# Optimization experiments

Hardware: AMD Instinct MI355X
Metric: run time of the kernel (lower is better)

Reference implementation:

```python
import jax, jax.numpy as jnp
import numpy as np

N, C, M, P, FL = 2, 512, 8, 1, 4
SPATIAL = [(100, 100), (50, 50), (25, 25), (13, 13)]
S = sum(h * w for h, w in SPATIAL)
CM = C // M


def grid_sample_zeros(im, grid):
    """torch.nn.functional.grid_sample, bilinear, padding_mode='zeros', align_corners=False.
    im: (B, Cc, H, W); grid: (B, Hg, Wg, 2) with grid[...,0]=x, grid[...,1]=y in [-1,1].
    Returns (B, Cc, Hg, Wg)."""
    B, Cc, H, W = im.shape
    Hg, Wg = grid.shape[1], grid.shape[2]
    x = (grid[..., 0] + 1.0) * (W * 0.5) - 0.5
    y = (grid[..., 1] + 1.0) * (H * 0.5) - 0.5
    x0f = jnp.floor(x)
    y0f = jnp.floor(y)
    wx1 = x - x0f
    wy1 = y - y0f
    wx0 = 1.0 - wx1
    wy0 = 1.0 - wy1
    x0 = x0f.astype(jnp.int32)
    y0 = y0f.astype(jnp.int32)
    flat = im.reshape(B, Cc, H * W)

    def gather(ix, iy):
        valid = ((ix >= 0) & (ix < W) & (iy >= 0) & (iy < H)).astype(im.dtype)
        idx = jnp.clip(iy, 0, H - 1) * W + jnp.clip(ix, 0, W - 1)  # (B,Hg,Wg)
        idx = jnp.broadcast_to(idx.reshape(B, 1, Hg * Wg), (B, Cc, Hg * Wg))
        v = jnp.take_along_axis(flat, idx, axis=2).reshape(B, Cc, Hg, Wg)
        return v * valid[:, None]

    out = (gather(x0, y0) * (wx0 * wy0)[:, None]
           + gather(x0 + 1, y0) * (wx1 * wy0)[:, None]
           + gather(x0, y0 + 1) * (wx0 * wy1)[:, None]
           + gather(x0 + 1, y0 + 1) * (wx1 * wy1)[:, None])
    return out


def setup_inputs() -> dict:
    key = jax.random.key(0)
    ks = jax.random.split(key, 8)
    x = jax.random.normal(ks[0], (N, C, S), jnp.float32)
    pos = jax.random.normal(ks[1], (N, C, S), jnp.float32)
    key_padding_mask = jnp.zeros((N, S), jnp.bool_)
    # valid (W,H) per level; no padding -> full size, scale 1
    valid_sizes = jnp.broadcast_to(
        jnp.array([[w, h] for (h, w) in SPATIAL], jnp.float32)[None], (N, FL, 2))
    valid_scales = jnp.ones((N, FL, 2), jnp.float32)
    s = 1.0 / np.sqrt(C)
    Wv = (jax.random.normal(ks[2], (C, C), jnp.float32) * s)
    bv = jnp.zeros((C,), jnp.float32)
    Wloc = jax.random.normal(ks[3], (M * FL * P * 2, C), jnp.float32) * 0.01
    # torch bias init: head-direction grid, channel layout (M, F, P, 2)
    grid_init = np.array([-1, -1, -1, 0, -1, 1, 0, -1, 0, 1, 1, -1, 1, 0, 1, 1],
                         np.float32).reshape(M, 1, 1, 2)
    grid_init = np.tile(grid_init, (1, FL, P, 1))
    for i in range(P):
        grid_init[:, :, i, :] *= (i + 1)
    bloc = jnp.asarray(grid_init.reshape(-1))
    Ww = jax.random.normal(ks[4], (M * FL * P, C), jnp.float32) * 0.01
    bw = jnp.zeros((M * FL * P,), jnp.float32)
    Wo = (jax.random.normal(ks[5], (C, C), jnp.float32) * s)
    bo = jnp.zeros((C,), jnp.float32)
    scale = jnp.ones((C,), jnp.float32)
    return dict(x=x, pos=pos, key_padding_mask=key_padding_mask,
                valid_sizes=valid_sizes, valid_scales=valid_scales,
                Wv=Wv, bv=bv, Wloc=Wloc, bloc=bloc, Ww=Ww, bw=bw,
                Wo=Wo, bo=bo, scale=scale)


def reference(x, pos, key_padding_mask, valid_sizes, valid_scales,
              Wv, bv, Wloc, bloc, Ww, bw, Wo, bo, scale):
    mask = key_padding_mask[:, None, :]  # (N,1,S)
    x_pos = jnp.where(mask, 0.0, x + pos)
    value = jnp.einsum('oc,ncs->nos', Wv, x) + bv[:, None]
    value = jnp.where(mask, 0.0, value)

    # per-level value maps, split heads: (N*M, C/M, H, W)
    values, cur = [], 0
    for (H, W) in SPATIAL:
        values.append(value[..., cur:cur + H * W].reshape(N * M, CM, H, W))
        cur += H * W

    vs = jnp.repeat(valid_sizes, M, axis=0)          # (NM, F, 2) = repeat_interleave
    vc2 = jnp.repeat(2.0 * valid_scales, M, axis=0)  # (NM, F, 2)

    outs, cur = [], 0
    for lvl, (H, W) in enumerate(SPATIAL):
        L = H * W
        xp = x_pos[..., cur:cur + L]  # (N, C, L)
        cur += L
        # 1x1 convs == per-token linears
        off = jnp.einsum('oc,ncl->nol', Wloc, xp) + bloc[:, None]
        off = off.reshape(N * M, FL, P, 2, L).transpose(0, 1, 2, 4, 3)  # (NM,F,P,L,2)
        w = jnp.einsum('oc,ncl->nol', Ww, xp) + bw[:, None]
        w = jax.nn.softmax(w.reshape(N * M, 1, FL * P, L), axis=2)
        # pixel-center grid of the query level, (L,2) as (x,y)
        ys, xs = jnp.meshgrid(jnp.arange(H, dtype=jnp.float32) + 0.5,
                              jnp.arange(W, dtype=jnp.float32) + 0.5, indexing='ij')
        pre = jnp.stack([xs, ys], -1).reshape(L, 2)
        sc = (vc2 / vs[:, lvl:lvl + 1])[:, :, None, None, :]  # (NM,F,1,1,2)
        grids = off * sc + (pre[None, None, None] * sc - 1.0)  # (NM,F,P,L,2)
        samples = jnp.concatenate(
            [grid_sample_zeros(values[f], grids[:, f]) for f in range(FL)], axis=2)  # (NM,CM,F*P,L)
        out = jnp.sum(samples * w, axis=2).reshape(N, C, L)
        out = jnp.einsum('oc,ncl->nol', Wo, out) + bo[:, None]
        outs.append(out)
    return jnp.concatenate(outs, axis=-1) * scale[None, :, None]
```

## Files before the change

### kernel.cpp

```cpp
#include <hip/hip_runtime.h>
#include <math.h>

#define TOT_S   13294
#define NBATCH  2
#define CCH     512
#define MHEAD   8
#define PITCH   40

typedef short     short8  __attribute__((ext_vector_type(8)));
typedef float     f32x4   __attribute__((ext_vector_type(4)));
typedef unsigned short u16x8 __attribute__((ext_vector_type(8)));
typedef unsigned short u16x4 __attribute__((ext_vector_type(4)));

__device__ __forceinline__ unsigned short f2bf(float f) {
    union { float f; unsigned int u; } v; v.f = f;
    unsigned int r = v.u + 0x7fffu + ((v.u >> 16) & 1u);
    return (unsigned short)(r >> 16);
}
__device__ __forceinline__ float bf2f(unsigned short h) {
    union { unsigned int u; float f; } v; v.u = ((unsigned int)h) << 16;
    return v.f;
}

__global__ void cast_f32_bf16(const float* __restrict__ src,
                              unsigned short* __restrict__ dst, int n4)
{
    const int i = blockIdx.x * blockDim.x + threadIdx.x;
    if (i < n4) {
        const float4 v = *(const float4*)(src + (size_t)i * 4);
        u16x4 o;
        o[0] = f2bf(v.x); o[1] = f2bf(v.y); o[2] = f2bf(v.z); o[3] = f2bf(v.w);
        *(u16x4*)(dst + (size_t)i * 4) = o;
    }
}

__global__ __launch_bounds__(256)
void cast_transpose(const float* __restrict__ x, const float* __restrict__ pos,
                    const unsigned char* __restrict__ mask,
                    unsigned short* __restrict__ xbt,
                    unsigned short* __restrict__ xpbt)
{
    const int lane = threadIdx.x;
    const int n = blockIdx.z;
    const int s = blockIdx.x * 64 + lane;
    if (s >= TOT_S) return;
    const int cb = (blockIdx.y * 4 + threadIdx.y) * 8;
    const float* xp = x   + ((size_t)n * CCH + cb) * TOT_S + s;
    const float* pp = pos + ((size_t)n * CCH + cb) * TOT_S + s;
    const bool mk = mask[(size_t)n * TOT_S + s] != 0;
    u16x8 vx, vp;
#pragma unroll
    for (int j = 0; j < 8; ++j) {
        const float a = xp[(size_t)j * TOT_S];
        const float b = pp[(size_t)j * TOT_S];
        vx[j] = f2bf(a);
        vp[j] = mk ? (unsigned short)0 : f2bf(a + b);
    }
    const size_t o = ((size_t)n * TOT_S + s) * CCH + cb;
    *(u16x8*)(xbt + o)  = vx;
    *(u16x8*)(xpbt + o) = vp;
}

__global__ __launch_bounds__(256)
void gemm_value_mfma(const unsigned short* __restrict__ Wb,
                     const unsigned short* __restrict__ Act,
                     const float* __restrict__ bv,
                     const unsigned char* __restrict__ mask,
                     unsigned short* __restrict__ valb)
{
    __shared__ unsigned short Wl[128 * PITCH];
    __shared__ unsigned short Al[128 * PITCH];
    const int n  = blockIdx.z;
    const int ob = blockIdx.y * 128;
    const int sb = blockIdx.x * 128;
    const int tid = threadIdx.x;
    const int r   = tid >> 1;
    const int seg = (tid & 1) * 16;
    const unsigned short* wsrc = Wb + ((size_t)(ob + r)) * CCH + seg;
    const int sr = min(sb + r, TOT_S - 1);
    const unsigned short* asrc = Act + ((size_t)n * TOT_S + sr) * CCH + seg;
    unsigned short* wdst = &Wl[r * PITCH + seg];
    unsigned short* adst = &Al[r * PITCH + seg];

    const int wave = tid >> 6, lane = tid & 63;
    const int m0 = (wave & 1) * 64, n0 = (wave >> 1) * 64;
    const int row16 = lane & 15, q = lane >> 4;

    u16x8 w0 = *(const u16x8*)(wsrc);
    u16x8 w1 = *(const u16x8*)(wsrc + 8);
    u16x8 a0 = *(const u16x8*)(asrc);
    u16x8 a1 = *(const u16x8*)(asrc + 8);

    f32x4 acc[4][4] = {};
    for (int k0 = 0; k0 < CCH; k0 += 32) {
        *(u16x8*)wdst = w0; *(u16x8*)(wdst + 8) = w1;
        *(u16x8*)adst = a0; *(u16x8*)(adst + 8) = a1;
        __syncthreads();
        if (k0 + 32 < CCH) {
            w0 = *(const u16x8*)(wsrc + k0 + 32);
            w1 = *(const u16x8*)(wsrc + k0 + 40);
            a0 = *(const u16x8*)(asrc + k0 + 32);
            a1 = *(const u16x8*)(asrc + k0 + 40);
        }
        short8 af[4], bfr[4];
#pragma unroll
        for (int mt = 0; mt < 4; ++mt)
            af[mt] = *(const short8*)&Wl[(m0 + mt * 16 + row16) * PITCH + q * 8];
#pragma unroll
        for (int nt = 0; nt < 4; ++nt)
            bfr[nt] = *(const short8*)&Al[(n0 + nt * 16 + row16) * PITCH + q * 8];
#pragma unroll
        for (int mt = 0; mt < 4; ++mt)
#pragma unroll
            for (int nt = 0; nt < 4; ++nt)
                acc[mt][nt] = __builtin_amdgcn_mfma_f32_16x16x32_bf16(
                    af[mt], bfr[nt], acc[mt][nt], 0, 0, 0);
        __syncthreads();
    }

#pragma unroll
    for (int nt = 0; nt < 4; ++nt) {
        const int s = sb + n0 + nt * 16 + row16;
        if (s >= TOT_S) continue;
        const float msk = mask[(size_t)n * TOT_S + s] ? 0.f : 1.f;
        unsigned short* orow = valb + ((size_t)n * TOT_S + s) * CCH + ob + m0;
#pragma unroll
        for (int mt = 0; mt < 4; ++mt) {
            const f32x4 bvv = *(const f32x4*)(bv + ob + m0 + mt * 16 + q * 4);
            const f32x4 a = acc[mt][nt];
            u16x4 ov;
            ov[0] = f2bf((a[0] + bvv[0]) * msk);
            ov[1] = f2bf((a[1] + bvv[1]) * msk);
            ov[2] = f2bf((a[2] + bvv[2]) * msk);
            ov[3] = f2bf((a[3] + bvv[3]) * msk);
            *(u16x4*)(orow + mt * 16 + q * 4) = ov;
        }
    }
}

__global__ __launch_bounds__(256)
void gemm_offw_mfma(const unsigned short* __restrict__ Wlb,
                    const unsigned short* __restrict__ Wwb,
                    const float* __restrict__ bloc, const float* __restrict__ bw,
                    const unsigned short* __restrict__ Act,
                    float* __restrict__ offw)
{
    __shared__ unsigned short Wl[128 * PITCH];
    __shared__ unsigned short Al[128 * PITCH];
    const int n  = blockIdx.z;
    const int sb = blockIdx.x * 128;
    const int tid = threadIdx.x;
    const int r   = tid >> 1;
    const int seg = (tid & 1) * 16;
    const bool wzero = (r >= 96);
    const unsigned short* wsrc =
        (r < 64) ? (Wlb + (size_t)r * CCH + seg)
                 : (Wwb + (size_t)((r < 96 ? r : 95) - 64) * CCH + seg);
    const int sr = min(sb + r, TOT_S - 1);
    const unsigned short* asrc = Act + ((size_t)n * TOT_S + sr) * CCH + seg;
    unsigned short* wdst = &Wl[r * PITCH + seg];
    unsigned short* adst = &Al[r * PITCH + seg];

    const int wave = tid >> 6, lane = tid & 63;
    const int m0 = (wave & 1) * 64, n0 = (wave >> 1) * 64;
    const int row16 = lane & 15, q = lane >> 4;

    u16x8 w0 = {}, w1 = {};
    if (!wzero) { w0 = *(const u16x8*)(wsrc); w1 = *(const u16x8*)(wsrc + 8); }
    u16x8 a0 = *(const u16x8*)(asrc);
    u16x8 a1 = *(const u16x8*)(asrc + 8);

    f32x4 acc[4][4] = {};
    for (int k0 = 0; k0 < CCH; k0 += 32) {
        *(u16x8*)wdst = w0; *(u16x8*)(wdst + 8) = w1;
        *(u16x8*)adst = a0; *(u16x8*)(adst + 8) = a1;
        __syncthreads();
        if (k0 + 32 < CCH) {
            if (!wzero) {
                w0 = *(const u16x8*)(wsrc + k0 + 32);
                w1 = *(const u16x8*)(wsrc + k0 + 40);
            }
            a0 = *(const u16x8*)(asrc + k0 + 32);
            a1 = *(const u16x8*)(asrc + k0 + 40);
        }
        short8 af[4], bfr[4];
#pragma unroll
        for (int mt = 0; mt < 4; ++mt)
            af[mt] = *(const short8*)&Wl[(m0 + mt * 16 + row16) * PITCH + q * 8];
#pragma unroll
        for (int nt = 0; nt < 4; ++nt)
            bfr[nt] = *(const short8*)&Al[(n0 + nt * 16 + row16) * PITCH + q * 8];
#pragma unroll
        for (int mt = 0; mt < 4; ++mt)
#pragma unroll
            for (int nt = 0; nt < 4; ++nt)
                acc[mt][nt] = __builtin_amdgcn_mfma_f32_16x16x32_bf16(
                    af[mt], bfr[nt], acc[mt][nt], 0, 0, 0);
        __syncthreads();
    }

#pragma unroll
    for (int nt = 0; nt < 4; ++nt) {
        const int s = sb + n0 + nt * 16 + row16;
        if (s >= TOT_S) continue;
        float* orow = offw + ((size_t)n * TOT_S + s) * 96;
#pragma unroll
        for (int mt = 0; mt < 4; ++mt) {
            const int o = m0 + mt * 16 + q * 4;
            if (o < 96) {
                const float* bsrc = (o < 64) ? (bloc + o) : (bw + o - 64);
                const f32x4 bb = *(const f32x4*)bsrc;
                f32x4 v = acc[mt][nt];
                v[0] += bb[0]; v[1] += bb[1]; v[2] += bb[2]; v[3] += bb[3];
                *(f32x4*)(orow + o) = v;
            }
        }
    }
}

__global__ __launch_bounds__(256)
void sample_attn(const unsigned short* __restrict__ value,
                 const float* __restrict__ offw,
                 const float* __restrict__ vsizes,
                 const float* __restrict__ vscales,
                 unsigned short* __restrict__ samp)
{
    const int lane = threadIdx.x;
    const int item = blockIdx.x * blockDim.y + threadIdx.y;
    const int total = NBATCH * TOT_S;
    if (item >= total) return;
    const int s = item % TOT_S;
    const int n = item / TOT_S;
    const int m = lane >> 3;

    int lvl; float prex, prey;
    if (s < 10000)      { lvl = 0; const int l = s;         const int qq = l / 100; prey = qq + 0.5f; prex = (l - qq * 100) + 0.5f; }
    else if (s < 12500) { lvl = 1; const int l = s - 10000; const int qq = l / 50;  prey = qq + 0.5f; prex = (l - qq * 50)  + 0.5f; }
    else if (s < 13125) { lvl = 2; const int l = s - 12500; const int qq = l / 25;  prey = qq + 0.5f; prex = (l - qq * 25)  + 0.5f; }
    else                { lvl = 3; const int l = s - 13125; const int qq = l / 13;  prey = qq + 0.5f; prex = (l - qq * 13)  + 0.5f; }

    const float* ow = offw + ((size_t)n * TOT_S + s) * 96;

    const float w0 = ow[64 + m * 4 + 0], w1 = ow[64 + m * 4 + 1];
    const float w2 = ow[64 + m * 4 + 2], w3 = ow[64 + m * 4 + 3];
    const float mx = fmaxf(fmaxf(w0, w1), fmaxf(w2, w3));
    const float e0 = expf(w0 - mx), e1 = expf(w1 - mx), e2 = expf(w2 - mx), e3 = expf(w3 - mx);
    const float inv = 1.f / (e0 + e1 + e2 + e3);
    const float wgt[4] = { e0 * inv, e1 * inv, e2 * inv, e3 * inv };

    const int HS[4]  = { 100, 50, 25, 13 };
    const int WS[4]  = { 100, 50, 25, 13 };
    const int CUR[4] = { 0, 10000, 12500, 13125 };

    const float invsx = 1.f / vsizes[((n * 4) + lvl) * 2 + 0];
    const float invsy = 1.f / vsizes[((n * 4) + lvl) * 2 + 1];
    const unsigned short* vbase = value + (size_t)n * TOT_S * CCH + lane * 8;

    float acc[8] = {};
#pragma unroll
    for (int f = 0; f < 4; ++f) {
        const float offx = ow[(m * 4 + f) * 2 + 0];
        const float offy = ow[(m * 4 + f) * 2 + 1];
        const float scx = 2.f * vscales[((n * 4) + f) * 2 + 0] * invsx;
        const float scy = 2.f * vscales[((n * 4) + f) * 2 + 1] * invsy;
        const int Wf = WS[f], Hf = HS[f], cf = CUR[f];
        const float xi = (offx + prex) * scx * (Wf * 0.5f) - 0.5f;
        const float yi = (offy + prey) * scy * (Hf * 0.5f) - 0.5f;
        const float x0f = floorf(xi), y0f = floorf(yi);
        const float wx1 = xi - x0f, wy1 = yi - y0f;
        const float wx0 = 1.f - wx1, wy0 = 1.f - wy1;
        const int x0 = (int)x0f, y0 = (int)y0f;
        const bool xin0 = (x0 >= 0) && (x0 < Wf);
        const bool xin1 = (x0 + 1 >= 0) && (x0 + 1 < Wf);
        const bool yin0 = (y0 >= 0) && (y0 < Hf);
        const bool yin1 = (y0 + 1 >= 0) && (y0 + 1 < Hf);
        const float cw00 = (xin0 && yin0) ? wgt[f] * wx0 * wy0 : 0.f;
        const float cw10 = (xin1 && yin0) ? wgt[f] * wx1 * wy0 : 0.f;
        const float cw01 = (xin0 && yin1) ? wgt[f] * wx0 * wy1 : 0.f;
        const float cw11 = (xin1 && yin1) ? wgt[f] * wx1 * wy1 : 0.f;
        const int x0c = min(max(x0, 0), Wf - 1);
        const int x1c = min(max(x0 + 1, 0), Wf - 1);
        const int y0c = min(max(y0, 0), Hf - 1);
        const int y1c = min(max(y0 + 1, 0), Hf - 1);
        const unsigned short* row0 = vbase + (size_t)(cf + y0c * Wf) * CCH;
        const unsigned short* row1 = vbase + (size_t)(cf + y1c * Wf) * CCH;
        const u16x8 v00 = *(const u16x8*)(row0 + (size_t)x0c * CCH);
        const u16x8 v10 = *(const u16x8*)(row0 + (size_t)x1c * CCH);
        const u16x8 v01 = *(const u16x8*)(row1 + (size_t)x0c * CCH);
        const u16x8 v11 = *(const u16x8*)(row1 + (size_t)x1c * CCH);
#pragma unroll
        for (int j = 0; j < 8; ++j) {
            acc[j] += cw00 * bf2f(v00[j]) + cw10 * bf2f(v10[j])
                    + cw01 * bf2f(v01[j]) + cw11 * bf2f(v11[j]);
        }
    }

    u16x8 ov;
#pragma unroll
    for (int j = 0; j < 8; ++j) ov[j] = f2bf(acc[j]);
    *(u16x8*)(samp + ((size_t)n * TOT_S + s) * CCH + lane * 8) = ov;
}

__global__ __launch_bounds__(256)
void gemm_out_mfma(const unsigned short* __restrict__ Wob,
                   const unsigned short* __restrict__ Sampb,
                   const float* __restrict__ bo, const float* __restrict__ scale,
                   float* __restrict__ out)
{
    __shared__ unsigned short Sl[128 * PITCH];
    __shared__ unsigned short Wl[128 * PITCH];
    const int n  = blockIdx.z;
    const int ob = blockIdx.y * 128;
    const int sb = blockIdx.x * 128;
    const int tid = threadIdx.x;
    const int r   = tid >> 1;
    const int seg = (tid & 1) * 16;
    const int sr = min(sb + r, TOT_S - 1);
    const unsigned short* ssrc = Sampb + ((size_t)n * TOT_S + sr) * CCH + seg;
    const unsigned short* wsrc = Wob + ((size_t)(ob + r)) * CCH + seg;
    unsigned short* sdst = &Sl[r * PITCH + seg];
    unsigned short* wdst = &Wl[r * PITCH + seg];

    const int wave = tid >> 6, lane = tid & 63;
    const int m0 = (wave & 1) * 64, n0 = (wave >> 1) * 64;
    const int row16 = lane & 15, q = lane >> 4;

    u16x8 s0v = *(const u16x8*)(ssrc);
    u16x8 s1v = *(const u16x8*)(ssrc + 8);
    u16x8 w0v = *(const u16x8*)(wsrc);
    u16x8 w1v = *(const u16x8*)(wsrc + 8);

    f32x4 acc[4][4] = {};
    for (int k0 = 0; k0 < CCH; k0 += 32) {
        *(u16x8*)sdst = s0v; *(u16x8*)(sdst + 8) = s1v;
        *(u16x8*)wdst = w0v; *(u16x8*)(wdst + 8) = w1v;
        __syncthreads();
        if (k0 + 32 < CCH) {
            s0v = *(const u16x8*)(ssrc + k0 + 32);
            s1v = *(const u16x8*)(ssrc + k0 + 40);
            w0v = *(const u16x8*)(wsrc + k0 + 32);
            w1v = *(const u16x8*)(wsrc + k0 + 40);
        }
        short8 af[4], bfr[4];
#pragma unroll
        for (int mt = 0; mt < 4; ++mt)
            af[mt] = *(const short8*)&Sl[(m0 + mt * 16 + row16) * PITCH + q * 8];
#pragma unroll
        for (int nt = 0; nt < 4; ++nt)
            bfr[nt] = *(const short8*)&Wl[(n0 + nt * 16 + row16) * PITCH + q * 8];
#pragma unroll
        for (int mt = 0; mt < 4; ++mt)
#pragma unroll
            for (int nt = 0; nt < 4; ++nt)
                acc[mt][nt] = __builtin_amdgcn_mfma_f32_16x16x32_bf16(
                    af[mt], bfr[nt], acc[mt][nt], 0, 0, 0);
        __syncthreads();
    }

#pragma unroll
    for (int nt = 0; nt < 4; ++nt) {
        const int o = ob + n0 + nt * 16 + row16;
        const float bo_ = bo[o];
        const float sc_ = scale[o];
        float* orow = out + ((size_t)n * CCH + o) * (size_t)TOT_S;
#pragma unroll
        for (int mt = 0; mt < 4; ++mt) {
            const int s0 = sb + m0 + mt * 16 + q * 4;
            const f32x4 a = acc[mt][nt];
            if (s0 + 3 < TOT_S) {
                float2 v0 = make_float2((a[0] + bo_) * sc_, (a[1] + bo_) * sc_);
                float2 v1 = make_float2((a[2] + bo_) * sc_, (a[3] + bo_) * sc_);
                *(float2*)(orow + s0) = v0;
                *(float2*)(orow + s0 + 2) = v1;
            } else {
                for (int i = 0; i < 4; ++i)
                    if (s0 + i < TOT_S) orow[s0 + i] = (a[i] + bo_) * sc_;
            }
        }
    }
}

extern "C" void kernel_launch(void* const* d_in, const int* in_sizes, int n_in,
                              void* d_out, int out_size, void* d_ws, size_t ws_size,
                              hipStream_t stream)
{
    const float* x     = (const float*)d_in[0];
    const float* pos   = (const float*)d_in[1];
    const unsigned char* mask = (const unsigned char*)d_in[2];
    const float* vsz   = (const float*)d_in[3];
    const float* vsc   = (const float*)d_in[4];
    const float* Wv    = (const float*)d_in[5];
    const float* bv    = (const float*)d_in[6];
    const float* Wloc  = (const float*)d_in[7];
    const float* bloc  = (const float*)d_in[8];
    const float* Ww    = (const float*)d_in[9];
    const float* bw    = (const float*)d_in[10];
    const float* Wo    = (const float*)d_in[11];
    const float* bo    = (const float*)d_in[12];
    const float* scale = (const float*)d_in[13];
    float* out = (float*)d_out;

    const size_t SC = (size_t)TOT_S * CCH;
    unsigned short* valb  = (unsigned short*)d_ws;
    unsigned short* sampb = valb  + 2 * SC;
    unsigned short* xbt   = sampb + 2 * SC;
    unsigned short* xpbt  = xbt   + 2 * SC;
    float* offw = (float*)(xpbt + 2 * SC);
    unsigned short* wvb = (unsigned short*)(offw + 2 * (size_t)TOT_S * 96);
    unsigned short* wob = wvb + 512 * 512;
    unsigned short* wlb = wob + 512 * 512;
    unsigned short* wwb = wlb + 64 * 512;

    cast_f32_bf16<<<256, 256, 0, stream>>>(Wv,   wvb, 512 * 512 / 4);
    cast_f32_bf16<<<256, 256, 0, stream>>>(Wo,   wob, 512 * 512 / 4);
    cast_f32_bf16<<<32,  256, 0, stream>>>(Wloc, wlb, 64 * 512 / 4);
    cast_f32_bf16<<<16,  256, 0, stream>>>(Ww,   wwb, 32 * 512 / 4);

    cast_transpose<<<dim3((TOT_S + 63) / 64, 16, NBATCH), dim3(64, 4), 0, stream>>>(
        x, pos, mask, xbt, xpbt);

    const int sTiles = (TOT_S + 127) / 128;

    gemm_value_mfma<<<dim3(sTiles, CCH / 128, NBATCH), 256, 0, stream>>>(
        wvb, xbt, bv, mask, valb);
    gemm_offw_mfma<<<dim3(sTiles, 1, NBATCH), 256, 0, stream>>>(
        wlb, wwb, bloc, bw, xpbt, offw);

    const int items = NBATCH * TOT_S;
    sample_attn<<<(items + 3) / 4, dim3(64, 4), 0, stream>>>(valb, offw, vsz, vsc, sampb);

    gemm_out_mfma<<<dim3(sTiles, CCH / 128, NBATCH), 256, 0, stream>>>(
        wob, sampb, bo, scale, out);
}
```

Baseline: 314.2 us.

## Fuse fp32-to-bf16 cast and transpose into value and offset GEMM loaders

Removes the separate cast_transpose kernel and has the value and offset/weight GEMMs read fp32 x and pos directly from channel-major layout. They convert to bf16 on the fly and transpose into shared memory. This drops the bf16 transposed intermediate buffers and their write/read round trip. The cost is that the value GEMM rereads fp32 x once per output-channel tile (4x), and the shared-memory stores are narrower and may bank-conflict.

```diff
diff --git a/kernel.cpp b/kernel.cpp
--- a/kernel.cpp
+++ b/kernel.cpp
@@ -35,35 +35,8 @@
 }
 
 __global__ __launch_bounds__(256)
-void cast_transpose(const float* __restrict__ x, const float* __restrict__ pos,
-                    const unsigned char* __restrict__ mask,
-                    unsigned short* __restrict__ xbt,
-                    unsigned short* __restrict__ xpbt)
-{
-    const int lane = threadIdx.x;
-    const int n = blockIdx.z;
-    const int s = blockIdx.x * 64 + lane;
-    if (s >= TOT_S) return;
-    const int cb = (blockIdx.y * 4 + threadIdx.y) * 8;
-    const float* xp = x   + ((size_t)n * CCH + cb) * TOT_S + s;
-    const float* pp = pos + ((size_t)n * CCH + cb) * TOT_S + s;
-    const bool mk = mask[(size_t)n * TOT_S + s] != 0;
-    u16x8 vx, vp;
-#pragma unroll
-    for (int j = 0; j < 8; ++j) {
-        const float a = xp[(size_t)j * TOT_S];
-        const float b = pp[(size_t)j * TOT_S];
-        vx[j] = f2bf(a);
-        vp[j] = mk ? (unsigned short)0 : f2bf(a + b);
-    }
-    const size_t o = ((size_t)n * TOT_S + s) * CCH + cb;
-    *(u16x8*)(xbt + o)  = vx;
-    *(u16x8*)(xpbt + o) = vp;
-}
-
-__global__ __launch_bounds__(256)
 void gemm_value_mfma(const unsigned short* __restrict__ Wb,
-                     const unsigned short* __restrict__ Act,
+                     const float* __restrict__ X,
                      const float* __restrict__ bv,
                      const unsigned char* __restrict__ mask,
                      unsigned short* __restrict__ valb)
@@ -74,13 +47,18 @@
     const int ob = blockIdx.y * 128;
     const int sb = blockIdx.x * 128;
     const int tid = threadIdx.x;
+
     const int r   = tid >> 1;
     const int seg = (tid & 1) * 16;
     const unsigned short* wsrc = Wb + ((size_t)(ob + r)) * CCH + seg;
-    const int sr = min(sb + r, TOT_S - 1);
-    const unsigned short* asrc = Act + ((size_t)n * TOT_S + sr) * CCH + seg;
     unsigned short* wdst = &Wl[r * PITCH + seg];
-    unsigned short* adst = &Al[r * PITCH + seg];
+
+    const int kr = tid & 7;
+    const int sq = tid >> 3;
+    const int sl = sq * 4;
+    const int sg = sb + sl;
+    const float* Xn = X + (size_t)n * CCH * TOT_S;
+    const bool fast = (sg + 3 < TOT_S);
 
     const int wave = tid >> 6, lane = tid & 63;
     const int m0 = (wave & 1) * 64, n0 = (wave >> 1) * 64;
@@ -88,19 +66,42 @@
 
     u16x8 w0 = *(const u16x8*)(wsrc);
     u16x8 w1 = *(const u16x8*)(wsrc + 8);
-    u16x8 a0 = *(const u16x8*)(asrc);
-    u16x8 a1 = *(const u16x8*)(asrc + 8);
+    f32x4 xv[4];
+#pragma unroll
+    for (int j = 0; j < 4; ++j) {
+        const size_t roff = (size_t)(kr * 4 + j) * TOT_S;
+        if (fast) xv[j] = *(const f32x4*)(Xn + roff + sg);
+        else {
+#pragma unroll
+            for (int i = 0; i < 4; ++i)
+                xv[j][i] = Xn[roff + min(sg + i, TOT_S - 1)];
+        }
+    }
 
     f32x4 acc[4][4] = {};
     for (int k0 = 0; k0 < CCH; k0 += 32) {
         *(u16x8*)wdst = w0; *(u16x8*)(wdst + 8) = w1;
-        *(u16x8*)adst = a0; *(u16x8*)(adst + 8) = a1;
+#pragma unroll
+        for (int i = 0; i < 4; ++i) {
+            u16x4 t;
+            t[0] = f2bf(xv[0][i]); t[1] = f2bf(xv[1][i]);
+            t[2] = f2bf(xv[2][i]); t[3] = f2bf(xv[3][i]);
+            *(u16x4*)&Al[(sl + i) * PITCH + kr * 4] = t;
+        }
         __syncthreads();
         if (k0 + 32 < CCH) {
             w0 = *(const u16x8*)(wsrc + k0 + 32);
             w1 = *(const u16x8*)(wsrc + k0 + 40);
-            a0 = *(const u16x8*)(asrc + k0 + 32);
-            a1 = *(const u16x8*)(asrc + k0 + 40);
+#pragma unroll
+            for (int j = 0; j < 4; ++j) {
+                const size_t roff = (size_t)(k0 + 32 + kr * 4 + j) * TOT_S;
+                if (fast) xv[j] = *(const f32x4*)(Xn + roff + sg);
+                else {
+#pragma unroll
+                    for (int i = 0; i < 4; ++i)
+                        xv[j][i] = Xn[roff + min(sg + i, TOT_S - 1)];
+                }
+            }
         }
         short8 af[4], bfr[4];
 #pragma unroll
@@ -142,7 +143,8 @@
 void gemm_offw_mfma(const unsigned short* __restrict__ Wlb,
                     const unsigned short* __restrict__ Wwb,
                     const float* __restrict__ bloc, const float* __restrict__ bw,
-                    const unsigned short* __restrict__ Act,
+                    const float* __restrict__ X, const float* __restrict__ POS,
+                    const unsigned char* __restrict__ mask,
                     float* __restrict__ offw)
 {
     __shared__ unsigned short Wl[128 * PITCH];
@@ -150,16 +152,26 @@
     const int n  = blockIdx.z;
     const int sb = blockIdx.x * 128;
     const int tid = threadIdx.x;
+
     const int r   = tid >> 1;
     const int seg = (tid & 1) * 16;
     const bool wzero = (r >= 96);
     const unsigned short* wsrc =
         (r < 64) ? (Wlb + (size_t)r * CCH + seg)
                  : (Wwb + (size_t)((r < 96 ? r : 95) - 64) * CCH + seg);
-    const int sr = min(sb + r, TOT_S - 1);
-    const unsigned short* asrc = Act + ((size_t)n * TOT_S + sr) * CCH + seg;
     unsigned short* wdst = &Wl[r * PITCH + seg];
-    unsigned short* adst = &Al[r * PITCH + seg];
+
+    const int kr = tid & 7;
+    const int sq = tid >> 3;
+    const int sl = sq * 4;
+    const int sg = sb + sl;
+    const float* Xn = X   + (size_t)n * CCH * TOT_S;
+    const float* Pn = POS + (size_t)n * CCH * TOT_S;
+    const bool fast = (sg + 3 < TOT_S);
+    float mkf[4];
+#pragma unroll
+    for (int i = 0; i < 4; ++i)
+        mkf[i] = mask[(size_t)n * TOT_S + min(sg + i, TOT_S - 1)] ? 0.f : 1.f;
 
     const int wave = tid >> 6, lane = tid & 63;
     const int m0 = (wave & 1) * 64, n0 = (wave >> 1) * 64;
@@ -167,21 +179,56 @@
 
     u16x8 w0 = {}, w1 = {};
     if (!wzero) { w0 = *(const u16x8*)(wsrc); w1 = *(const u16x8*)(wsrc + 8); }
-    u16x8 a0 = *(const u16x8*)(asrc);
-    u16x8 a1 = *(const u16x8*)(asrc + 8);
+    f32x4 xv[4];
+#pragma unroll
+    for (int j = 0; j < 4; ++j) {
+        const size_t roff = (size_t)(kr * 4 + j) * TOT_S;
+        if (fast) {
+            const f32x4 a = *(const f32x4*)(Xn + roff + sg);
+            const f32x4 b = *(const f32x4*)(Pn + roff + sg);
+#pragma unroll
+            for (int i = 0; i < 4; ++i) xv[j][i] = (a[i] + b[i]) * mkf[i];
+        } else {
+#pragma unroll
+            for (int i = 0; i < 4; ++i) {
+                const int si = min(sg + i, TOT_S - 1);
+                xv[j][i] = (Xn[roff + si] + Pn[roff + si]) * mkf[i];
+            }
+        }
+    }
 
     f32x4 acc[4][4] = {};
     for (int k0 = 0; k0 < CCH; k0 += 32) {
         *(u16x8*)wdst = w0; *(u16x8*)(wdst + 8) = w1;
-        *(u16x8*)adst = a0; *(u16x8*)(adst + 8) = a1;
+#pragma unroll
+        for (int i = 0; i < 4; ++i) {
+            u16x4 t;
+            t[0] = f2bf(xv[0][i]); t[1] = f2bf(xv[1][i]);
+            t[2] = f2bf(xv[2][i]); t[3] = f2bf(xv[3][i]);
+            *(u16x4*)&Al[(sl + i) * PITCH + kr * 4] = t;
+        }
         __syncthreads();
         if (k0 + 32 < CCH) {
             if (!wzero) {
                 w0 = *(const u16x8*)(wsrc + k0 + 32);
                 w1 = *(const u16x8*)(wsrc + k0 + 40);
             }
-            a0 = *(const u16x8*)(asrc + k0 + 32);
-            a1 = *(const u16x8*)(asrc + k0 + 40);
+#pragma unroll
+            for (int j = 0; j < 4; ++j) {
+                const size_t roff = (size_t)(k0 + 32 + kr * 4 + j) * TOT_S;
+                if (fast) {
+                    const f32x4 a = *(const f32x4*)(Xn + roff + sg);
+                    const f32x4 b = *(const f32x4*)(Pn + roff + sg);
+#pragma unroll
+                    for (int i = 0; i < 4; ++i) xv[j][i] = (a[i] + b[i]) * mkf[i];
+                } else {
+#pragma unroll
+                    for (int i = 0; i < 4; ++i) {
+                        const int si = min(sg + i, TOT_S - 1);
+                        xv[j][i] = (Xn[roff + si] + Pn[roff + si]) * mkf[i];
+                    }
+                }
+            }
         }
         short8 af[4], bfr[4];
 #pragma unroll
@@ -403,9 +450,7 @@
     const size_t SC = (size_t)TOT_S * CCH;
     unsigned short* valb  = (unsigned short*)d_ws;
     unsigned short* sampb = valb  + 2 * SC;
-    unsigned short* xbt   = sampb + 2 * SC;
-    unsigned short* xpbt  = xbt   + 2 * SC;
-    float* offw = (float*)(xpbt + 2 * SC);
+    float* offw = (float*)(sampb + 2 * SC);
     unsigned short* wvb = (unsigned short*)(offw + 2 * (size_t)TOT_S * 96);
     unsigned short* wob = wvb + 512 * 512;
     unsigned short* wlb = wob + 512 * 512;
@@ -416,15 +461,12 @@
     cast_f32_bf16<<<32,  256, 0, stream>>>(Wloc, wlb, 64 * 512 / 4);
     cast_f32_bf16<<<16,  256, 0, stream>>>(Ww,   wwb, 32 * 512 / 4);
 
-    cast_transpose<<<dim3((TOT_S + 63) / 64, 16, NBATCH), dim3(64, 4), 0, stream>>>(
-        x, pos, mask, xbt, xpbt);
-
     const int sTiles = (TOT_S + 127) / 128;
 
     gemm_value_mfma<<<dim3(sTiles, CCH / 128, NBATCH), 256, 0, stream>>>(
-        wvb, xbt, bv, mask, valb);
+        wvb, x, bv, mask, valb);
     gemm_offw_mfma<<<dim3(sTiles, 1, NBATCH), 256, 0, stream>>>(
-        wlb, wwb, bloc, bw, xpbt, offw);
+        wlb, wwb, bloc, bw, x, pos, mask, offw);
 
     const int items = NBATCH * TOT_S;
     sample_attn<<<(items + 3) / 4, dim3(64, 4), 0, stream>>>(valb, offw, vsz, vsc, sampb);
```

New measurement: 349.1 us. +11.1%, slower.
